# Kernel tuning notes

Measured on AMD Instinct MI355X. Metric: run time of the kernel, lower is better.

The kernel has to match this reference:

```python
import jax, jax.numpy as jnp
from jax import lax
import numpy as np


def _conv(x, w):
    # x: [B,Cin,H,W], w: [Cout,Cin,kh,kw] -> [B,Cout,H,W], SAME padding
    return lax.conv_general_dilated(x, w, (1, 1), 'SAME')


def setup_inputs() -> dict:
    key = jax.random.key(0)
    ks = jax.random.split(key, 16)
    B, Hh, W = 8, 256, 256
    inputs = jax.random.normal(ks[0], (B, Hh, W), jnp.float32)
    H0 = jax.random.normal(ks[1], (B, Hh, W), jnp.float32)
    C0 = jax.random.normal(ks[2], (B, 2, Hh, W), jnp.float32)
    # learned scalars: c2 ~ U(0,1), sf ~ N(0, 0.01) shifted away from 0 (it is a divisor)
    c2 = jax.random.uniform(ks[3], (1,), jnp.float32, 0.0, 1.0)
    sf = 0.01 * jax.random.normal(ks[4], (1,), jnp.float32) + 0.02
    # RedNet (assumed small conv encoder-decoder): 1->32->64->32->1, 3x3 SAME, ReLU
    w1 = 0.1 * jax.random.normal(ks[5], (32, 1, 3, 3), jnp.float32)
    b1 = jnp.zeros((32,), jnp.float32)
    w2 = 0.1 * jax.random.normal(ks[6], (64, 32, 3, 3), jnp.float32)
    b2 = jnp.zeros((64,), jnp.float32)
    w3 = 0.1 * jax.random.normal(ks[7], (32, 64, 3, 3), jnp.float32)
    b3 = jnp.zeros((32,), jnp.float32)
    w4 = 0.1 * jax.random.normal(ks[8], (1, 32, 3, 3), jnp.float32)
    b4 = jnp.zeros((1,), jnp.float32)
    return dict(inputs=inputs, H0=H0, C0=C0, c2=c2, sf=sf,
                w1=w1, b1=b1, w2=w2, b2=b2, w3=w3, b3=b3, w4=w4, b4=b4)


def reference(inputs, H0, C0, c2, sf, w1, b1, w2, b2, w3, b3, w4, b4):
    # Fixed 5-point Laplacian stencil (non-trainable in the original module)
    lap_k = jnp.array([[0., 1., 0.], [1., -4., 1.], [0., 1., 0.]],
                      dtype=inputs.dtype)[None, None]  # [1,1,3,3]

    # torch chain: C' = permute/matmul(Wcc^T)/permute + wcu*U
    #   reduces exactly to: C'[:,0] = inputs, C'[:,1] = C_old[:,0]
    C_new = jnp.stack([inputs, C0[:, 0]], axis=1)  # [B,2,H,W]

    V = inputs - H0  # [B,H,W]

    # H = whc . C' = 2*C'[:,0] - C'[:,1] = 2*inputs - C_old[:,0]
    lap = _conv(inputs[:, None], lap_k)[:, 0]  # [B,H,W]
    H = 2.0 * inputs - C0[:, 0] + c2 * lap

    # RedNet on scaled residual V
    h = (V / sf)[:, None]  # [B,1,H,W]
    h = jax.nn.relu(_conv(h, w1) + b1[None, :, None, None])
    h = jax.nn.relu(_conv(h, w2) + b2[None, :, None, None])
    h = jax.nn.relu(_conv(h, w3) + b3[None, :, None, None])
    V_hat = (_conv(h, w4) + b4[None, :, None, None])[:, 0] * sf  # [B,H,W]

    outputs = H + V_hat
    return (outputs, H, C_new, V, V_hat)
```

## Files before the change

### kernel.cpp

```cpp
#include <hip/hip_runtime.h>

#define PLANE 65536
#define WIDTH 256
#define PADW 258
#define PADPLANE 66564

typedef __bf16 v8bf __attribute__((ext_vector_type(8)));
typedef float  v4f  __attribute__((ext_vector_type(4)));

typedef const __attribute__((address_space(1))) unsigned int* gas_ptr;
typedef __attribute__((address_space(3))) unsigned int* las_ptr;

__device__ __forceinline__ void gl_lds(const void* g, void* l) {
  __builtin_amdgcn_global_load_lds((gas_ptr)g, (las_ptr)l, 16, 0, 0);
}

__device__ __forceinline__ int swz(int c) {
  return (c & ~7) | ((c & 7) ^ ((c >> 3) & 7));
}

__device__ __forceinline__ int m6(int x) { return x >= 6 ? x - 6 : x; }

__device__ __forceinline__ unsigned int pack2(float a, float b) {
  __bf16 ba = (__bf16)a, bb = (__bf16)b;
  unsigned short sa = __builtin_bit_cast(unsigned short, ba);
  unsigned short sb = __builtin_bit_cast(unsigned short, bb);
  return (unsigned int)sa | ((unsigned int)sb << 16);
}

#define WT_N 37440
#define ZR_N (8 * 1028 * 32)
__global__ __launch_bounds__(256) void wz_k(
    const float* __restrict__ w1, const float* __restrict__ w2,
    const float* __restrict__ w3, const float* __restrict__ w4,
    float* __restrict__ w1t, __bf16* __restrict__ B2t,
    __bf16* __restrict__ B3t, float* __restrict__ w4t,
    __bf16* __restrict__ a1, __bf16* __restrict__ a3)
{
  int t = blockIdx.x * 256 + threadIdx.x;
  if (t < WT_N) {
    if (t < 288) {
      int tap = t >> 5, cout = t & 31;
      w1t[t] = w1[cout * 9 + tap];
    }
    int t2 = t - 288;
    if (t2 >= 0 && t2 < 18432) {
      int cout = t2 / 288, k = t2 % 288;
      int tap = k / 32, cin = k % 32;
      B2t[t2] = (__bf16)w2[cout * 288 + cin * 9 + tap];
    }
    int t3 = t - (288 + 18432);
    if (t3 >= 0 && t3 < 18432) {
      int cout = t3 / 576, k = t3 % 576;
      int tap = k / 64, cin = k % 64;
      B3t[t3] = (__bf16)w3[cout * 576 + cin * 9 + tap];
    }
    int t4 = t - (288 + 18432 + 18432);
    if (t4 >= 0 && t4 < 288) {
      int tap = t4 >> 5, cin = t4 & 31;
      w4t[t4] = w4[cin * 9 + tap];
    }
    return;
  }
  int idx = t - WT_N;
  if (idx >= ZR_N) return;
  unsigned int* p;
  const int R1 = 8 * 1028 * 16;
  if (idx < R1) p = (unsigned int*)a1;
  else         { p = (unsigned int*)a3; idx -= R1; }
  int ch = idx & 15;
  int pr = idx >> 4;
  int b = pr / 1028, r = pr % 1028;
  int y, x;
  if      (r < 258) { y = 0;           x = r; }
  else if (r < 516) { y = 257;         x = r - 258; }
  else if (r < 772) { y = r - 516 + 1; x = 0; }
  else              { y = r - 772 + 1; x = 257; }
  p[((size_t)b * PADPLANE + y * PADW + x) * 16 + ch] = 0;
}

__global__ __launch_bounds__(256) void prepconv1_k(
    const float* __restrict__ inputs, const float* __restrict__ H0,
    const float* __restrict__ C0, const float* __restrict__ c2p,
    const float* __restrict__ sfp, const float* __restrict__ w1t,
    const float* __restrict__ b1, float* __restrict__ dout,
    __bf16* __restrict__ act1)
{
  const int x = threadIdx.x, y = blockIdx.x, b = blockIdx.y;
  const int p = b * PLANE + y * WIDTH + x;
  const float c2 = c2p[0], sf = sfp[0], rsf = 1.0f / sf;

  float iv[3][3], hv[3][3];
  #pragma unroll
  for (int dy = 0; dy < 3; dy++) {
    int yy = y + dy - 1;
    #pragma unroll
    for (int dx = 0; dx < 3; dx++) {
      int xx = x + dx - 1;
      bool ok = (yy >= 0 && yy < 256 && xx >= 0 && xx < 256);
      int pn = p + (dy - 1) * WIDTH + (dx - 1);
      iv[dy][dx] = ok ? inputs[pn] : 0.f;
      hv[dy][dx] = ok ? H0[pn]     : 0.f;
    }
  }
  const float in = iv[1][1], h0 = hv[1][1];
  const float c0a = C0[b * 131072 + y * WIDTH + x];
  float lap = iv[0][1] + iv[2][1] + iv[1][0] + iv[1][2] - 4.f * in;
  float Hv = 2.f * in - c0a + c2 * lap;
  float V  = in - h0;
  dout[524288 + p]  = Hv;
  dout[2097152 + p] = V;
  dout[1048576 + b * 131072 + y * WIDTH + x]         = in;
  dout[1048576 + b * 131072 + 65536 + y * WIDTH + x] = c0a;

  float acc[32];
  #pragma unroll
  for (int i = 0; i < 32; i++) acc[i] = b1[i];
  #pragma unroll
  for (int tap = 0; tap < 9; tap++) {
    float v = (iv[tap / 3][tap % 3] - hv[tap / 3][tap % 3]) * rsf;
    const float* wp = w1t + tap * 32;
    #pragma unroll
    for (int i = 0; i < 32; i++) acc[i] = fmaf(wp[i], v, acc[i]);
  }
  unsigned int u[16];
  #pragma unroll
  for (int j = 0; j < 16; j++)
    u[j] = pack2(fmaxf(acc[2*j], 0.f), fmaxf(acc[2*j+1], 0.f));
  size_t pa = ((size_t)b * PADPLANE + (y+1) * PADW + (x+1)) * 32;
  uint4* op = reinterpret_cast<uint4*>(act1 + pa);
  #pragma unroll
  for (int j = 0; j < 4; j++)
    op[j] = make_uint4(u[4*j], u[4*j+1], u[4*j+2], u[4*j+3]);
}

#define A1ROWB 4352
#define A2ROWB 8448
__global__ __launch_bounds__(256, 2) void conv23_k(
    const __bf16* __restrict__ act1, const __bf16* __restrict__ B2t,
    const float* __restrict__ b2, const __bf16* __restrict__ B3t,
    const float* __restrict__ b3, __bf16* __restrict__ act3)
{
  const int lane = threadIdx.x & 63, wave = threadIdx.x >> 6;
  const int l15 = lane & 15, q = lane >> 4;
  const int y0 = blockIdx.x * 16, xt = blockIdx.y, b = blockIdx.z;
  const int x0 = xt * 64;
  __shared__ __align__(16) char smem[6 * A2ROWB + 6 * A1ROWB + 1024];
  char* a2r = smem;
  char* a1r = smem + 6 * A2ROWB;
  const __bf16* plane = act1 + (size_t)b * PADPLANE * 32;

  auto stageA1 = [&](int k, int slot) {
    int a = y0 - 1 + k;
    a = a < 0 ? 0 : (a > 257 ? 257 : a);
    const char* g = (const char*)(plane + ((size_t)a * PADW + x0 - 1) * 32);
    char* lrow = a1r + slot * A1ROWB;
    const int base = wave * 68;
    gl_lds(g + (size_t)swz(base + lane) * 16, lrow + base * 16);
    if (lane < 4)
      gl_lds(g + (size_t)swz(base + 64 + lane) * 16, lrow + (base + 64) * 16);
  };

  v8bf breg2[9];
  #pragma unroll
  for (int tap = 0; tap < 9; tap++)
    breg2[tap] = *(const v8bf*)(B2t + (size_t)(wave * 16 + l15) * 288
                                    + tap * 32 + q * 8);
  const v4f bv2 = *(const v4f*)(b2 + wave * 16 + q * 4);

  const int Mh = wave >> 1, ntw = wave & 1;
  v8bf breg3[9][2];
  #pragma unroll
  for (int tap = 0; tap < 9; tap++)
    #pragma unroll
    for (int kb = 0; kb < 2; kb++)
      breg3[tap][kb] = *(const v8bf*)(B3t + (size_t)(ntw * 16 + l15) * 576
                                          + tap * 64 + kb * 32 + q * 8);
  const float bv3 = b3[ntw * 16 + l15];

  auto produce = [&](int t, int s) {
    char* drow = a2r + s * A2ROWB;
    int pr = y0 + t;
    if (pr == 0 || pr == 257) {
      int c = threadIdx.x;
      *(uint4*)(drow + (size_t)c * 16)         = make_uint4(0,0,0,0);
      *(uint4*)(drow + (size_t)(c + 256) * 16) = make_uint4(0,0,0,0);
      if (c < 16)
        *(uint4*)(drow + (size_t)(c + 512) * 16) = make_uint4(0,0,0,0);
      return;
    }
    v4f acc[5];
    #pragma unroll
    for (int m = 0; m < 5; m++) acc[m] = bv2;
    #pragma unroll
    for (int tap = 0; tap < 9; tap++) {
      const int dy = tap / 3, dx = tap % 3;
      const char* srow = a1r + m6(s + dy) * A1ROWB;
      #pragma unroll
      for (int m = 0; m < 5; m++) {
        int j = m * 16 + l15 + dx;
        v8bf af = *(const v8bf*)(srow + (size_t)swz(j * 4 + q) * 16);
        acc[m] = __builtin_amdgcn_mfma_f32_16x16x32_bf16(
            breg2[tap], af, acc[m], 0, 0, 0);
      }
    }
    const int c = wave * 2 + (q >> 1), boff = (q & 1) * 8;
    #pragma unroll
    for (int m = 0; m < 5; m++) {
      int px = m * 16 + l15;
      bool w = (m < 4) || (l15 < 2);
      if (x0 == 0   && px == 0)  w = false;
      if (x0 == 192 && px == 65) w = false;
      if (w) {
        unsigned int lo = pack2(fmaxf(acc[m][0], 0.f), fmaxf(acc[m][1], 0.f));
        unsigned int hi = pack2(fmaxf(acc[m][2], 0.f), fmaxf(acc[m][3], 0.f));
        *(uint2*)(drow + (size_t)swz(px * 8 + c) * 16 + boff)
            = make_uint2(lo, hi);
      }
    }
    if (x0 == 0 && threadIdx.x < 8)
      *(uint4*)(drow + (size_t)swz(threadIdx.x) * 16) = make_uint4(0,0,0,0);
    if (x0 == 192 && threadIdx.x < 8)
      *(uint4*)(drow + (size_t)swz(520 + threadIdx.x) * 16) = make_uint4(0,0,0,0);
  };

  #pragma unroll
  for (int k = 0; k < 6; k++) stageA1(k, k);
  asm volatile("s_waitcnt vmcnt(0)" ::: "memory");
  __builtin_amdgcn_s_barrier();
  __builtin_amdgcn_sched_barrier(0);
  produce(0, 0);
  produce(1, 1);
  asm volatile("s_waitcnt lgkmcnt(0)" ::: "memory");
  __builtin_amdgcn_s_barrier();
  __builtin_amdgcn_sched_barrier(0);

  int sb = 0;
  for (int ps = 0; ps < 8; ps++) {
    if (2 * ps + 6 <= 19) stageA1(2 * ps + 6, sb);
    if (2 * ps + 7 <= 19) stageA1(2 * ps + 7, m6(sb + 1));

    produce(2 * ps + 2, m6(sb + 2));
    produce(2 * ps + 3, m6(sb + 3));
    asm volatile("s_waitcnt lgkmcnt(0)" ::: "memory");
    __builtin_amdgcn_s_barrier();
    __builtin_amdgcn_sched_barrier(0);

    {
      v4f acc3[2][2];
      #pragma unroll
      for (int rr = 0; rr < 2; rr++)
        #pragma unroll
        for (int mt = 0; mt < 2; mt++)
          acc3[rr][mt] = (v4f){bv3, bv3, bv3, bv3};

      __builtin_amdgcn_s_setprio(1);
      #pragma unroll
      for (int t = 0; t < 4; t++) {
        const char* srow = a2r + m6(sb + t) * A2ROWB;
        #pragma unroll
        for (int dx = 0; dx < 3; dx++) {
          #pragma unroll
          for (int kb = 0; kb < 2; kb++) {
            v8bf af[2];
            #pragma unroll
            for (int mt = 0; mt < 2; mt++) {
              int P = Mh * 32 + mt * 16 + l15 + dx;
              af[mt] = *(const v8bf*)(srow + (size_t)swz(P * 8 + kb * 4 + q) * 16);
            }
            #pragma unroll
            for (int mt = 0; mt < 2; mt++) {
              if (t <= 2)
                acc3[0][mt] = __builtin_amdgcn_mfma_f32_16x16x32_bf16(
                    af[mt], breg3[t * 3 + dx][kb], acc3[0][mt], 0, 0, 0);
              if (t >= 1)
                acc3[1][mt] = __builtin_amdgcn_mfma_f32_16x16x32_bf16(
                    af[mt], breg3[(t - 1) * 3 + dx][kb], acc3[1][mt], 0, 0, 0);
            }
          }
        }
      }
      __builtin_amdgcn_s_setprio(0);

      #pragma unroll
      for (int rr = 0; rr < 2; rr++) {
        size_t rb = ((size_t)b * PADPLANE
                     + (size_t)(y0 + 2 * ps + rr + 1) * PADW + x0 + 1) * 32;
        #pragma unroll
        for (int mt = 0; mt < 2; mt++) {
          #pragma unroll
          for (int r = 0; r < 4; r++) {
            int px = Mh * 32 + mt * 16 + q * 4 + r;
            act3[rb + (size_t)px * 32 + ntw * 16 + l15] =
                (__bf16)fmaxf(acc3[rr][mt][r], 0.f);
          }
        }
      }
    }
    asm volatile("s_waitcnt vmcnt(16)" ::: "memory");
    __builtin_amdgcn_s_barrier();
    __builtin_amdgcn_sched_barrier(0);
    sb = m6(sb + 2);
  }
}

#define C4ROWB 16512
__global__ __launch_bounds__(256, 2) void conv4_k(
    const __bf16* __restrict__ act3, const float* __restrict__ w4t,
    const float* __restrict__ b4, const float* __restrict__ sfp,
    float* __restrict__ dout)
{
  const int x = threadIdx.x, lane = threadIdx.x & 63, wave = threadIdx.x >> 6;
  const int y0 = blockIdx.x * 2, b = blockIdx.y;
  const float b4v = b4[0], sf = sfp[0];
  const __bf16* plane = act3 + (size_t)b * PADPLANE * 32;
  __shared__ __align__(16) char smem[4 * C4ROWB];

  #pragma unroll
  for (int r = 0; r < 4; r++) {
    const char* g = (const char*)(plane + (size_t)(y0 + r) * PADW * 32);
    char* lrow = smem + r * C4ROWB;
    #pragma unroll
    for (int k = 0; k < 4; k++) {
      int c = k * 256 + wave * 64 + lane;
      gl_lds(g + (size_t)swz(c) * 16, lrow + (k * 256 + wave * 64) * 16);
    }
    if (wave == 0 && lane < 8) {
      int c = 1024 + lane;
      gl_lds(g + (size_t)swz(c) * 16, lrow + 1024 * 16);
    }
  }
  asm volatile("s_waitcnt vmcnt(0)" ::: "memory");
  __builtin_amdgcn_s_barrier();

  float acc0 = b4v, acc1 = b4v;
  #pragma unroll
  for (int t = 0; t < 4; t++) {
    const char* srow = smem + t * C4ROWB;
    uint4 L[12];
    #pragma unroll
    for (int j = 0; j < 12; j++) {
      int chunk = (x + (j >> 2)) * 4 + (j & 3);
      L[j] = *(const uint4*)(srow + (size_t)swz(chunk) * 16);
    }
    #pragma unroll
    for (int j = 0; j < 12; j++) {
      const int dx = j >> 2, c0 = (j & 3) * 8;
      unsigned int uu[4] = {L[j].x, L[j].y, L[j].z, L[j].w};
      float f[8];
      #pragma unroll
      for (int k = 0; k < 4; k++) {
        f[2*k]   = __builtin_bit_cast(float, uu[k] << 16);
        f[2*k+1] = __builtin_bit_cast(float, uu[k] & 0xFFFF0000u);
      }
      if (t <= 2) {
        const float* wp = w4t + (t * 3 + dx) * 32 + c0;
        #pragma unroll
        for (int k = 0; k < 8; k++) acc0 = fmaf(wp[k], f[k], acc0);
      }
      if (t >= 1) {
        const float* wp = w4t + ((t - 1) * 3 + dx) * 32 + c0;
        #pragma unroll
        for (int k = 0; k < 8; k++) acc1 = fmaf(wp[k], f[k], acc1);
      }
    }
  }
  size_t p0 = ((size_t)b << 16) + (size_t)y0 * WIDTH + x;
  float vh0 = acc0 * sf, vh1 = acc1 * sf;
  dout[p0]                   = dout[524288 + p0] + vh0;
  dout[2621440 + p0]         = vh0;
  dout[p0 + WIDTH]           = dout[524288 + p0 + WIDTH] + vh1;
  dout[2621440 + p0 + WIDTH] = vh1;
}

extern "C" void kernel_launch(void* const* d_in, const int* in_sizes, int n_in,
                              void* d_out, int out_size, void* d_ws, size_t ws_size,
                              hipStream_t stream) {
  const float* inputs = (const float*)d_in[0];
  const float* H0     = (const float*)d_in[1];
  const float* C0     = (const float*)d_in[2];
  const float* c2     = (const float*)d_in[3];
  const float* sf     = (const float*)d_in[4];
  const float* w1     = (const float*)d_in[5];
  const float* b1     = (const float*)d_in[6];
  const float* w2     = (const float*)d_in[7];
  const float* b2     = (const float*)d_in[8];
  const float* w3     = (const float*)d_in[9];
  const float* b3     = (const float*)d_in[10];
  const float* w4     = (const float*)d_in[11];
  const float* b4     = (const float*)d_in[12];
  float* out = (float*)d_out;
  float* ws  = (float*)d_ws;

  float*  w1t  = ws;
  float*  w4t  = ws + 288;
  __bf16* B2t  = (__bf16*)(ws + 576);
  __bf16* B3t  = (__bf16*)(ws + 9792);
  __bf16* act1 = (__bf16*)(ws + 19008);
  __bf16* act3 = act1 + (size_t)8 * PADPLANE * 32;

  wz_k<<<1175, 256, 0, stream>>>(w1, w2, w3, w4, w1t, B2t, B3t, w4t,
                                 act1, act3);
  prepconv1_k<<<dim3(256, 8), 256, 0, stream>>>(inputs, H0, C0, c2, sf,
                                                w1t, b1, out, act1);
  conv23_k<<<dim3(16, 4, 8), 256, 0, stream>>>(act1, B2t, b2, B3t, b3, act3);
  conv4_k<<<dim3(128, 8), 256, 0, stream>>>(act3, w4t, b4, sf, out);
}
```

Measured before the change: 172.7 us.

## Warp-specialize conv23 into producer conv2 waves and consumer conv3 waves

Doubles the conv23 block to 512 threads. Four waves now only stage act1 rows and compute conv2 rows into the LDS ring, running two rows ahead. The other four waves only compute conv3 from that ring and store act3, with matched barriers keeping the two groups in step. The goal is to overlap conv2 production with conv3 consumption and global loads instead of running them in series within each wave. Launch bounds are raised to 512 threads with 4 blocks per CU, which tightens the per-thread register budget and could force spills of the preloaded weight registers.

```diff
diff --git a/kernel.cpp b/kernel.cpp
--- a/kernel.cpp
+++ b/kernel.cpp
@@ -136,7 +136,7 @@
 
 #define A1ROWB 4352
 #define A2ROWB 8448
-__global__ __launch_bounds__(256, 2) void conv23_k(
+__global__ __launch_bounds__(512, 4) void conv23_k(
     const __bf16* __restrict__ act1, const __bf16* __restrict__ B2t,
     const float* __restrict__ b2, const __bf16* __restrict__ B3t,
     const float* __restrict__ b3, __bf16* __restrict__ act3)
@@ -150,103 +150,115 @@
   char* a1r = smem + 6 * A2ROWB;
   const __bf16* plane = act1 + (size_t)b * PADPLANE * 32;
 
-  auto stageA1 = [&](int k, int slot) {
-    int a = y0 - 1 + k;
-    a = a < 0 ? 0 : (a > 257 ? 257 : a);
-    const char* g = (const char*)(plane + ((size_t)a * PADW + x0 - 1) * 32);
-    char* lrow = a1r + slot * A1ROWB;
-    const int base = wave * 68;
-    gl_lds(g + (size_t)swz(base + lane) * 16, lrow + base * 16);
-    if (lane < 4)
-      gl_lds(g + (size_t)swz(base + 64 + lane) * 16, lrow + (base + 64) * 16);
-  };
-
-  v8bf breg2[9];
-  #pragma unroll
-  for (int tap = 0; tap < 9; tap++)
-    breg2[tap] = *(const v8bf*)(B2t + (size_t)(wave * 16 + l15) * 288
-                                    + tap * 32 + q * 8);
-  const v4f bv2 = *(const v4f*)(b2 + wave * 16 + q * 4);
-
-  const int Mh = wave >> 1, ntw = wave & 1;
-  v8bf breg3[9][2];
-  #pragma unroll
-  for (int tap = 0; tap < 9; tap++)
-    #pragma unroll
-    for (int kb = 0; kb < 2; kb++)
-      breg3[tap][kb] = *(const v8bf*)(B3t + (size_t)(ntw * 16 + l15) * 576
-                                          + tap * 64 + kb * 32 + q * 8);
-  const float bv3 = b3[ntw * 16 + l15];
-
-  auto produce = [&](int t, int s) {
-    char* drow = a2r + s * A2ROWB;
-    int pr = y0 + t;
-    if (pr == 0 || pr == 257) {
-      int c = threadIdx.x;
-      *(uint4*)(drow + (size_t)c * 16)         = make_uint4(0,0,0,0);
-      *(uint4*)(drow + (size_t)(c + 256) * 16) = make_uint4(0,0,0,0);
-      if (c < 16)
-        *(uint4*)(drow + (size_t)(c + 512) * 16) = make_uint4(0,0,0,0);
-      return;
-    }
-    v4f acc[5];
-    #pragma unroll
-    for (int m = 0; m < 5; m++) acc[m] = bv2;
-    #pragma unroll
-    for (int tap = 0; tap < 9; tap++) {
-      const int dy = tap / 3, dx = tap % 3;
-      const char* srow = a1r + m6(s + dy) * A1ROWB;
+  if (wave < 4) {
+    auto stageA1 = [&](int k, int slot) {
+      int a = y0 - 1 + k;
+      a = a < 0 ? 0 : (a > 257 ? 257 : a);
+      const char* g = (const char*)(plane + ((size_t)a * PADW + x0 - 1) * 32);
+      char* lrow = a1r + slot * A1ROWB;
+      const int base = wave * 68;
+      gl_lds(g + (size_t)swz(base + lane) * 16, lrow + base * 16);
+      if (lane < 4)
+        gl_lds(g + (size_t)swz(base + 64 + lane) * 16, lrow + (base + 64) * 16);
+    };
+
+    v8bf breg2[9];
+    #pragma unroll
+    for (int tap = 0; tap < 9; tap++)
+      breg2[tap] = *(const v8bf*)(B2t + (size_t)(wave * 16 + l15) * 288
+                                      + tap * 32 + q * 8);
+    const v4f bv2 = *(const v4f*)(b2 + wave * 16 + q * 4);
+
+    auto produce = [&](int t, int s) {
+      char* drow = a2r + s * A2ROWB;
+      int pr = y0 + t;
+      if (pr == 0 || pr == 257) {
+        int c = threadIdx.x;
+        *(uint4*)(drow + (size_t)c * 16)         = make_uint4(0,0,0,0);
+        *(uint4*)(drow + (size_t)(c + 256) * 16) = make_uint4(0,0,0,0);
+        if (c < 16)
+          *(uint4*)(drow + (size_t)(c + 512) * 16) = make_uint4(0,0,0,0);
+        return;
+      }
+      v4f acc[5];
+      #pragma unroll
+      for (int m = 0; m < 5; m++) acc[m] = bv2;
+      #pragma unroll
+      for (int tap = 0; tap < 9; tap++) {
+        const int dy = tap / 3, dx = tap % 3;
+        const char* srow = a1r + m6(s + dy) * A1ROWB;
+        #pragma unroll
+        for (int m = 0; m < 5; m++) {
+          int j = m * 16 + l15 + dx;
+          v8bf af = *(const v8bf*)(srow + (size_t)swz(j * 4 + q) * 16);
+          acc[m] = __builtin_amdgcn_mfma_f32_16x16x32_bf16(
+              breg2[tap], af, acc[m], 0, 0, 0);
+        }
+      }
+      const int c = wave * 2 + (q >> 1), boff = (q & 1) * 8;
       #pragma unroll
       for (int m = 0; m < 5; m++) {
-        int j = m * 16 + l15 + dx;
-        v8bf af = *(const v8bf*)(srow + (size_t)swz(j * 4 + q) * 16);
-        acc[m] = __builtin_amdgcn_mfma_f32_16x16x32_bf16(
-            breg2[tap], af, acc[m], 0, 0, 0);
-      }
-    }
-    const int c = wave * 2 + (q >> 1), boff = (q & 1) * 8;
-    #pragma unroll
-    for (int m = 0; m < 5; m++) {
-      int px = m * 16 + l15;
-      bool w = (m < 4) || (l15 < 2);
-      if (x0 == 0   && px == 0)  w = false;
-      if (x0 == 192 && px == 65) w = false;
-      if (w) {
-        unsigned int lo = pack2(fmaxf(acc[m][0], 0.f), fmaxf(acc[m][1], 0.f));
-        unsigned int hi = pack2(fmaxf(acc[m][2], 0.f), fmaxf(acc[m][3], 0.f));
-        *(uint2*)(drow + (size_t)swz(px * 8 + c) * 16 + boff)
-            = make_uint2(lo, hi);
-      }
-    }
-    if (x0 == 0 && threadIdx.x < 8)
-      *(uint4*)(drow + (size_t)swz(threadIdx.x) * 16) = make_uint4(0,0,0,0);
-    if (x0 == 192 && threadIdx.x < 8)
-      *(uint4*)(drow + (size_t)swz(520 + threadIdx.x) * 16) = make_uint4(0,0,0,0);
-  };
-
-  #pragma unroll
-  for (int k = 0; k < 6; k++) stageA1(k, k);
-  asm volatile("s_waitcnt vmcnt(0)" ::: "memory");
-  __builtin_amdgcn_s_barrier();
-  __builtin_amdgcn_sched_barrier(0);
-  produce(0, 0);
-  produce(1, 1);
-  asm volatile("s_waitcnt lgkmcnt(0)" ::: "memory");
-  __builtin_amdgcn_s_barrier();
-  __builtin_amdgcn_sched_barrier(0);
-
-  int sb = 0;
-  for (int ps = 0; ps < 8; ps++) {
-    if (2 * ps + 6 <= 19) stageA1(2 * ps + 6, sb);
-    if (2 * ps + 7 <= 19) stageA1(2 * ps + 7, m6(sb + 1));
-
-    produce(2 * ps + 2, m6(sb + 2));
-    produce(2 * ps + 3, m6(sb + 3));
+        int px = m * 16 + l15;
+        bool w = (m < 4) || (l15 < 2);
+        if (x0 == 0   && px == 0)  w = false;
+        if (x0 == 192 && px == 65) w = false;
+        if (w) {
+          unsigned int lo = pack2(fmaxf(acc[m][0], 0.f), fmaxf(acc[m][1], 0.f));
+          unsigned int hi = pack2(fmaxf(acc[m][2], 0.f), fmaxf(acc[m][3], 0.f));
+          *(uint2*)(drow + (size_t)swz(px * 8 + c) * 16 + boff)
+              = make_uint2(lo, hi);
+        }
+      }
+      if (x0 == 0 && threadIdx.x < 8)
+        *(uint4*)(drow + (size_t)swz(threadIdx.x) * 16) = make_uint4(0,0,0,0);
+      if (x0 == 192 && threadIdx.x < 8)
+        *(uint4*)(drow + (size_t)swz(520 + threadIdx.x) * 16) = make_uint4(0,0,0,0);
+    };
+
+    #pragma unroll
+    for (int k = 0; k < 6; k++) stageA1(k, k);
+    asm volatile("s_waitcnt vmcnt(0)" ::: "memory");
+    __builtin_amdgcn_s_barrier();
+    __builtin_amdgcn_sched_barrier(0);
+    produce(0, 0); produce(1, 1); produce(2, 2); produce(3, 3);
     asm volatile("s_waitcnt lgkmcnt(0)" ::: "memory");
     __builtin_amdgcn_s_barrier();
     __builtin_amdgcn_sched_barrier(0);
-
-    {
+    stageA1(6, 0); stageA1(7, 1);
+    asm volatile("s_waitcnt vmcnt(0)" ::: "memory");
+    __builtin_amdgcn_s_barrier();
+    __builtin_amdgcn_sched_barrier(0);
+
+    int sb = 2;
+    for (int ps = 0; ps < 8; ps++) {
+      int r0 = 2 * ps + 8, r1 = 2 * ps + 9;
+      stageA1(r0 > 19 ? 19 : r0, sb);
+      stageA1(r1 > 19 ? 19 : r1, m6(sb + 1));
+      if (2 * ps + 4 <= 17) produce(2 * ps + 4, m6(sb + 2));
+      if (2 * ps + 5 <= 17) produce(2 * ps + 5, m6(sb + 3));
+      asm volatile("s_waitcnt vmcnt(0) lgkmcnt(0)" ::: "memory");
+      __builtin_amdgcn_s_barrier();
+      __builtin_amdgcn_sched_barrier(0);
+      sb = m6(sb + 2);
+    }
+  } else {
+    const int cw = wave - 4;
+    const int Mh = cw >> 1, ntw = cw & 1;
+    v8bf breg3[9][2];
+    #pragma unroll
+    for (int tap = 0; tap < 9; tap++)
+      #pragma unroll
+      for (int kb = 0; kb < 2; kb++)
+        breg3[tap][kb] = *(const v8bf*)(B3t + (size_t)(ntw * 16 + l15) * 576
+                                            + tap * 64 + kb * 32 + q * 8);
+    const float bv3 = b3[ntw * 16 + l15];
+
+    __builtin_amdgcn_s_barrier();
+    __builtin_amdgcn_s_barrier();
+    __builtin_amdgcn_s_barrier();
+
+    int sc = 0;
+    for (int ps = 0; ps < 8; ps++) {
       v4f acc3[2][2];
       #pragma unroll
       for (int rr = 0; rr < 2; rr++)
@@ -257,7 +269,7 @@
       __builtin_amdgcn_s_setprio(1);
       #pragma unroll
       for (int t = 0; t < 4; t++) {
-        const char* srow = a2r + m6(sb + t) * A2ROWB;
+        const char* srow = a2r + m6(sc + t) * A2ROWB;
         #pragma unroll
         for (int dx = 0; dx < 3; dx++) {
           #pragma unroll
@@ -296,11 +308,10 @@
           }
         }
       }
-    }
-    asm volatile("s_waitcnt vmcnt(16)" ::: "memory");
-    __builtin_amdgcn_s_barrier();
-    __builtin_amdgcn_sched_barrier(0);
-    sb = m6(sb + 2);
+      __builtin_amdgcn_s_barrier();
+      __builtin_amdgcn_sched_barrier(0);
+      sc = m6(sc + 2);
+    }
   }
 }
 
@@ -403,6 +414,6 @@
                                  act1, act3);
   prepconv1_k<<<dim3(256, 8), 256, 0, stream>>>(inputs, H0, C0, c2, sf,
                                                 w1t, b1, out, act1);
-  conv23_k<<<dim3(16, 4, 8), 256, 0, stream>>>(act1, B2t, b2, B3t, b3, act3);
+  conv23_k<<<dim3(16, 4, 8), 512, 0, stream>>>(act1, B2t, b2, B3t, b3, act3);
   conv4_k<<<dim3(128, 8), 256, 0, stream>>>(act3, w4t, b4, sf, out);
 }
```

After: 164.5 us. 1.05x faster.
